# Performance work log

Hardware: AMD Instinct MI355X
Metric: run time of the kernel (lower is better)

The kernel has to match this reference:

```python
import jax, jax.numpy as jnp
import numpy as np

KSIZE = 3
COUT = 128
GC = 4

def _unfold(x, k):
    # x: [B,C,H,W] -> [B,C,k*k,H,W]; zero pad (k-1)//2, stride 1 (matches nn.Unfold ordering)
    B, C, H, W = x.shape
    p = (k - 1) // 2
    xp = jnp.pad(x, ((0, 0), (0, 0), (p, p), (p, p)))
    return jnp.stack([xp[:, :, i:i + H, j:j + W] for i in range(k) for j in range(k)], axis=2)

def _bn(x, g, b, m, v, eps=1e-5):
    # inference-mode BatchNorm along channel axis 1, any rank
    sh = (1, -1) + (1,) * (x.ndim - 2)
    return (x - m.reshape(sh)) * (g / jnp.sqrt(v + eps)).reshape(sh) + b.reshape(sh)

def setup_inputs():
    key = jax.random.key(0)
    ks = jax.random.split(key, 15)
    B, C, H, W = 4, 128, 56, 56
    mid = C // 4
    OG = COUT * GC
    s = 0.05
    return {
        'x': jax.random.normal(ks[0], (B, C, H, W), jnp.float32),
        'Wk': jax.random.normal(ks[1], (C, C), jnp.float32) * s,
        'bn1_g': jax.random.uniform(ks[2], (C,), jnp.float32, 0.5, 1.5),
        'bn1_b': jax.random.normal(ks[3], (C,), jnp.float32) * s,
        'bn1_m': jnp.zeros((C,), jnp.float32),
        'bn1_v': jnp.ones((C,), jnp.float32),
        'W1': jax.random.normal(ks[4], (mid, 2 * C), jnp.float32) * s,
        'b1': jax.random.normal(ks[5], (mid,), jnp.float32) * s,
        'bn2_g': jax.random.uniform(ks[6], (mid,), jnp.float32, 0.5, 1.5),
        'bn2_b': jax.random.normal(ks[7], (mid,), jnp.float32) * s,
        'bn2_m': jnp.zeros((mid,), jnp.float32),
        'bn2_v': jnp.ones((mid,), jnp.float32),
        'W2': jax.random.normal(ks[8], (OG, mid), jnp.float32) * s,
        'b2': jax.random.normal(ks[9], (OG,), jnp.float32) * s,
        'gn_g': jax.random.uniform(ks[10], (OG,), jnp.float32, 0.5, 1.5),
        'gn_b': jax.random.normal(ks[11], (OG,), jnp.float32) * s,
        'Wv': jax.random.normal(ks[12], (OG, C), jnp.float32) * s,
        'bnv_g': jax.random.uniform(ks[13], (OG,), jnp.float32, 0.5, 1.5),
        'bnv_b': jax.random.normal(ks[14], (OG,), jnp.float32) * s,
        'bnv_m': jnp.zeros((OG,), jnp.float32),
        'bnv_v': jnp.ones((OG,), jnp.float32),
    }

def reference(x, Wk, bn1_g, bn1_b, bn1_m, bn1_v, W1, b1, bn2_g, bn2_b, bn2_m, bn2_v,
              W2, b2, gn_g, gn_b, Wv, bnv_g, bnv_b, bnv_m, bnv_v):
    B, C, H, W = x.shape
    k2 = KSIZE * KSIZE
    # emb_K: 1x1 conv (no bias) + BN + ReLU, then local unfold
    ke = jax.nn.relu(_bn(jnp.einsum('bchw,dc->bdhw', x, Wk), bn1_g, bn1_b, bn1_m, bn1_v))
    Kp = _unfold(ke, KSIZE)                        # [B,C,k2,H,W]
    Q = jnp.broadcast_to(x[:, :, None], Kp.shape)  # repeat x over k2 (einops '(c k)')
    QK = jnp.concatenate([Q, Kp], axis=1)          # [B,2C,k2,H,W]
    # MLP: 1x1 convs act pointwise over (k2,H,W)
    h = jax.nn.relu(_bn(jnp.einsum('bcphw,mc->bmphw', QK, W1) + b1.reshape(1, -1, 1, 1, 1),
                        bn2_g, bn2_b, bn2_m, bn2_v))
    a = jnp.einsum('bmphw,om->bophw', h, W2) + b2.reshape(1, -1, 1, 1, 1)  # [B,COUT*GC,k2,H,W]
    a = a.reshape(B, COUT, GC, k2, H, W)
    # GroupNorm: num_groups=COUT -> normalize over (GC, k2, H, W) per (b, out)
    mu = a.mean(axis=(2, 3, 4, 5), keepdims=True)
    var = jnp.mean(jnp.square(a - mu), axis=(2, 3, 4, 5), keepdims=True)
    a = (a - mu) / jnp.sqrt(var + 1e-5)
    a = a * gn_g.reshape(1, COUT, GC, 1, 1, 1) + gn_b.reshape(1, COUT, GC, 1, 1, 1)
    # emb_V: 1x1 conv (no bias) + BN, then local unfold
    v = _bn(jnp.einsum('bchw,oc->bohw', x, Wv), bnv_g, bnv_b, bnv_m, bnv_v)
    V = _unfold(v, KSIZE).reshape(B, COUT, GC, k2, H, W)
    return jnp.sum(a * V, axis=(2, 3))             # [B,COUT,H,W]
```

## Files before the change

kernel.cpp:

```cpp
#include <hip/hip_runtime.h>
#include <hip/hip_bf16.h>

typedef __hip_bfloat16 bf16;
typedef __attribute__((ext_vector_type(8))) short short8;
typedef __attribute__((ext_vector_type(4))) float f32x4;

#define HWP 3136
#define WD 56
#define PW 58
#define PADP 3364
#define CC 128
#define MIDM 32
#define OGN 512
#define NB 4

enum : int {
  OFF_FLAG = 0,
  OFF_W2F  = 4,
  OFF_SC2  = OFF_W2F + OGN*MIDM,
  OFF_SH2  = OFF_SC2 + MIDM,
  OFF_B1F  = OFF_SH2 + MIDM,
  OFF_B2F  = OFF_B1F + MIDM,
  OFF_GNG  = OFF_B2F + OGN,
  OFF_GNB  = OFF_GNG + OGN,
  OFF_GPART= OFF_GNB + OGN,
  OFF_PQ   = OFF_GPART + NB*128*1056,
  OFF_SS1  = OFF_PQ + NB*OGN*2,
  OFF_SSV  = OFF_SS1 + CC*2,
  OFF_WKB  = OFF_SSV + OGN*2,
  OFF_WVB  = OFF_WKB + CC*CC/2,
  OFF_W1AB = OFF_WVB + OGN*CC/2,
  OFF_W1BB = OFF_W1AB + MIDM*CC/2,
  OFF_HQT  = OFF_W1BB + MIDM*CC/2,
  OFF_GKT  = OFF_HQT + NB*HWP*MIDM/2,
  OFF_VT   = OFF_GKT + NB*PADP*MIDM/2,
  OFF_R1   = OFF_VT + NB*PADP*OGN/2,
  OFF_XT   = OFF_R1,
  OFF_AB   = OFF_R1,
  WS_TOTAL = OFF_R1 + NB*9*HWP*MIDM/2
};

__device__ __forceinline__ float b2f(unsigned short u) {
  bf16 h; *(unsigned short*)&h = u; return __bfloat162float(h);
}
__device__ __forceinline__ unsigned short f2b(float f) {
  bf16 h = __float2bfloat16(f); return *(unsigned short*)&h;
}
__device__ __forceinline__ float ldmix(const void* p, size_t i, bool isbf) {
  return isbf ? __bfloat162float(((const bf16*)p)[i]) : ((const float*)p)[i];
}
__device__ __forceinline__ f32x4 mfma16(short8 a, short8 b, f32x4 c) {
  return __builtin_amdgcn_mfma_f32_16x16x32_bf16(a, b, c, 0, 0, 0);
}
__device__ __forceinline__ bool detect_bf(const unsigned short* xr) {
  int cnt = 0;
#pragma unroll
  for (int i = 0; i < 32; i++) {
    short8 v = *(const short8*)(xr + i*8);
#pragma unroll
    for (int j = 0; j < 8; j++) {
      int e = (((unsigned short)v[j]) >> 7) & 0xFF;
      cnt += (e >= 141) ? 1 : 0;
    }
  }
  return cnt < 8;
}

__global__ __launch_bounds__(256) void k_prep(
    const void* __restrict__ x,  const void* __restrict__ Wk,
    const void* __restrict__ bn1_g, const void* __restrict__ bn1_b,
    const void* __restrict__ bn1_m, const void* __restrict__ bn1_v,
    const void* __restrict__ W1, const void* __restrict__ b1,
    const void* __restrict__ bn2_g, const void* __restrict__ bn2_b,
    const void* __restrict__ bn2_m, const void* __restrict__ bn2_v,
    const void* __restrict__ W2, const void* __restrict__ b2,
    const void* __restrict__ gn_g, const void* __restrict__ gn_b,
    const void* __restrict__ Wv,
    const void* __restrict__ bnv_g, const void* __restrict__ bnv_b,
    const void* __restrict__ bnv_m, const void* __restrict__ bnv_v,
    float* __restrict__ ws) {
  __shared__ unsigned short tile[32*130];
  const bool isbf = detect_bf((const unsigned short*)x);
  int blk = blockIdx.x, tid = threadIdx.x;
  if (blk == 0 && tid == 0) ws[OFF_FLAG] = isbf ? 1.f : 0.f;
  int gid = blk*256 + tid, gstride = gridDim.x*256;
  unsigned short* wkb = (unsigned short*)(ws + OFF_WKB);
  unsigned short* wvb = (unsigned short*)(ws + OFF_WVB);
  unsigned short* w1ab = (unsigned short*)(ws + OFF_W1AB);
  unsigned short* w1bb = (unsigned short*)(ws + OFF_W1BB);
  float2* ss1 = (float2*)(ws + OFF_SS1);
  float2* ssv = (float2*)(ws + OFF_SSV);
  for (int i = gid; i < CC*CC; i += gstride) wkb[i] = f2b(ldmix(Wk, i, isbf));
  for (int i = gid; i < OGN*CC; i += gstride) wvb[i] = f2b(ldmix(Wv, i, isbf));
  for (int i = gid; i < MIDM*CC; i += gstride) {
    int m = i / CC, c = i % CC;
    w1ab[i] = f2b(ldmix(W1, (size_t)m*(2*CC) + c, isbf));
    w1bb[i] = f2b(ldmix(W1, (size_t)m*(2*CC) + CC + c, isbf));
  }
  for (int i = gid; i < OGN*MIDM; i += gstride) ws[OFF_W2F + i] = ldmix(W2, i, isbf);
  for (int i = gid; i < CC; i += gstride) {
    float s = ldmix(bn1_g, i, isbf) / sqrtf(ldmix(bn1_v, i, isbf) + 1e-5f);
    ss1[i] = make_float2(s, ldmix(bn1_b, i, isbf) - ldmix(bn1_m, i, isbf) * s);
  }
  for (int i = gid; i < MIDM; i += gstride) {
    float s = ldmix(bn2_g, i, isbf) / sqrtf(ldmix(bn2_v, i, isbf) + 1e-5f);
    ws[OFF_SC2 + i] = s;
    ws[OFF_SH2 + i] = ldmix(bn2_b, i, isbf) - ldmix(bn2_m, i, isbf)*s;
    ws[OFF_B1F + i] = ldmix(b1, i, isbf);
  }
  for (int i = gid; i < OGN; i += gstride) {
    float s = ldmix(bnv_g, i, isbf) / sqrtf(ldmix(bnv_v, i, isbf) + 1e-5f);
    ssv[i] = make_float2(s, ldmix(bnv_b, i, isbf) - ldmix(bnv_m, i, isbf) * s);
    ws[OFF_B2F + i] = ldmix(b2, i, isbf);
    ws[OFF_GNG + i] = ldmix(gn_g, i, isbf);
    ws[OFF_GNB + i] = ldmix(gn_b, i, isbf);
  }
  if (blk < 392) {
    int b = blk / 98, pix0 = (blk % 98)*32;
#pragma unroll
    for (int k = 0; k < 16; k++) {
      int idx = tid + k*256;
      int c = idx >> 5, pl = idx & 31;
      tile[pl*130 + c] = f2b(ldmix(x, ((size_t)b*CC + c)*HWP + pix0 + pl, isbf));
    }
    __syncthreads();
    unsigned short* xt = (unsigned short*)(ws + OFF_XT);
#pragma unroll
    for (int k = 0; k < 16; k++) {
      int idx = tid + k*256;
      int c = idx & 127, pl = idx >> 7;
      xt[((size_t)b*HWP + pix0 + pl)*CC + c] = tile[pl*130 + c];
    }
  } else {
    const int NV = 912*64, NG = NB*PADP*4;
    const short8 z = {0,0,0,0,0,0,0,0};
    unsigned short* vt = (unsigned short*)(ws + OFF_VT);
    unsigned short* gk = (unsigned short*)(ws + OFF_GKT);
    for (int u = (blk-392)*256 + tid; u < NV + NG; u += 28*256) {
      if (u < NV) {
        int bpp = u >> 6, och = u & 63;
        int b = bpp / 228, j = bpp - b*228;
        int pp;
        if (j < 58)       pp = j;
        else if (j < 116) pp = 57*PW + (j - 58);
        else if (j < 172) pp = (j - 116 + 1)*PW;
        else              pp = (j - 172 + 1)*PW + 57;
        *(short8*)(vt + ((size_t)b*PADP + pp)*OGN + och*8) = z;
      } else {
        int u2 = u - NV;
        int b = u2 / (PADP*4), rem = u2 - b*(PADP*4);
        int pp = rem >> 2, mch = rem & 3;
        *(short8*)(gk + ((size_t)b*PADP + pp)*MIDM + mch*8) = z;
      }
    }
  }
}

__global__ __launch_bounds__(256, 4) void k_mid(float* __restrict__ ws) {
  __shared__ unsigned short keL[4][16][136];
  int bid = blockIdx.x, tid = threadIdx.x;
  int w = tid >> 6, lane = tid & 63, q = lane >> 4, l16 = lane & 15;
  if (bid < 196) {
    int b = bid / 49, bx = bid - (bid/49)*49;
    int pix = bx*64 + w*16 + l16;
    const unsigned short* xt = (const unsigned short*)(ws + OFF_XT) + ((size_t)b*HWP + pix)*CC;
    short8 Bx[4];
#pragma unroll
    for (int kk = 0; kk < 4; kk++) Bx[kk] = *(const short8*)(xt + kk*32 + q*8);
    const unsigned short* wkb = (const unsigned short*)(ws + OFF_WKB);
    const float2* ss = (const float2*)(ws + OFF_SS1);
#pragma unroll
    for (int ot = 0; ot < 8; ot++) {
      int drow = ot*16 + l16;
      f32x4 c = {0.f, 0.f, 0.f, 0.f};
#pragma unroll
      for (int kk = 0; kk < 4; kk++)
        c = mfma16(*(const short8*)(wkb + (size_t)drow*CC + kk*32 + q*8), Bx[kk], c);
      int d0 = ot*16 + q*4;
      ushort4 st;
      { float2 s = ss[d0+0]; st.x = f2b(fmaxf(s.x*c[0] + s.y, 0.f)); }
      { float2 s = ss[d0+1]; st.y = f2b(fmaxf(s.x*c[1] + s.y, 0.f)); }
      { float2 s = ss[d0+2]; st.z = f2b(fmaxf(s.x*c[2] + s.y, 0.f)); }
      { float2 s = ss[d0+3]; st.w = f2b(fmaxf(s.x*c[3] + s.y, 0.f)); }
      *(ushort4*)&keL[w][l16][d0] = st;
    }
    __syncthreads();
    short8 Bk[4];
#pragma unroll
    for (int kk = 0; kk < 4; kk++) Bk[kk] = *(const short8*)&keL[w][l16][kk*32 + q*8];
    const unsigned short* w1a = (const unsigned short*)(ws + OFF_W1AB);
    const unsigned short* w1b = (const unsigned short*)(ws + OFF_W1BB);
    int h0 = pix / WD, w0 = pix - h0*WD;
    int pp = (h0+1)*PW + (w0+1);
    unsigned short* hqt = (unsigned short*)(ws + OFF_HQT) + ((size_t)b*HWP + pix)*MIDM;
    unsigned short* gkt = (unsigned short*)(ws + OFF_GKT) + ((size_t)b*PADP + pp)*MIDM;
#pragma unroll
    for (int mt = 0; mt < 2; mt++) {
      int mrow = mt*16 + l16;
      f32x4 ch = {0.f,0.f,0.f,0.f}, cg = {0.f,0.f,0.f,0.f};
#pragma unroll
      for (int kk = 0; kk < 4; kk++) {
        ch = mfma16(*(const short8*)(w1a + (size_t)mrow*CC + kk*32 + q*8), Bx[kk], ch);
        cg = mfma16(*(const short8*)(w1b + (size_t)mrow*CC + kk*32 + q*8), Bk[kk], cg);
      }
      int m0 = mt*16 + q*4;
      ushort4 sh, sg;
      sh.x = f2b(ch[0]); sh.y = f2b(ch[1]); sh.z = f2b(ch[2]); sh.w = f2b(ch[3]);
      sg.x = f2b(cg[0]); sg.y = f2b(cg[1]); sg.z = f2b(cg[2]); sg.w = f2b(cg[3]);
      *(ushort4*)(hqt + m0) = sh;
      *(ushort4*)(gkt + m0) = sg;
    }
  } else {
    int vid = bid - 196;
    int bx = vid % 49, rest = vid / 49;
    int by = rest & 3, b = rest >> 2;
    int pix = bx*64 + w*16 + l16;
    int h0 = pix / WD, w0 = pix - h0*WD;
    int pp = (h0+1)*PW + (w0+1);
    const unsigned short* xt = (const unsigned short*)(ws + OFF_XT) + ((size_t)b*HWP + pix)*CC;
    short8 B[4];
#pragma unroll
    for (int kk = 0; kk < 4; kk++) B[kk] = *(const short8*)(xt + kk*32 + q*8);
    const unsigned short* wvb = (const unsigned short*)(ws + OFF_WVB);
    const float2* ss = (const float2*)(ws + OFF_SSV);
    unsigned short* vt = (unsigned short*)(ws + OFF_VT) + ((size_t)b*PADP + pp)*OGN;
#pragma unroll
    for (int ot = 0; ot < 8; ot++) {
      int orow = by*128 + ot*16 + l16;
      f32x4 c = {0.f, 0.f, 0.f, 0.f};
#pragma unroll
      for (int kk = 0; kk < 4; kk++)
        c = mfma16(*(const short8*)(wvb + (size_t)orow*CC + kk*32 + q*8), B[kk], c);
      int o0 = by*128 + ot*16 + q*4;
      ushort4 st;
      { float2 s = ss[o0+0]; st.x = f2b(s.x*c[0] + s.y); }
      { float2 s = ss[o0+1]; st.y = f2b(s.x*c[1] + s.y); }
      { float2 s = ss[o0+2]; st.z = f2b(s.x*c[2] + s.y); }
      { float2 s = ss[o0+3]; st.w = f2b(s.x*c[3] + s.y); }
      *(ushort4*)(vt + o0) = st;
    }
  }
}

__global__ __launch_bounds__(256) void k_gramh(float* __restrict__ ws) {
  __shared__ unsigned short tileT[32][264];
  int b = blockIdx.y, bk = blockIdx.x;
  int tid = threadIdx.x;
  int w = tid >> 6, lane = tid & 63, q = lane >> 4, l16 = lane & 15;
  const int base = bk * 882;
  const unsigned short* hqt = (const unsigned short*)(ws + OFF_HQT) + (size_t)b*HWP*MIDM;
  const unsigned short* gkp = (const unsigned short*)(ws + OFF_GKT) + (size_t)b*PADP*MIDM;
  float sc2[MIDM], bas0[MIDM];
#pragma unroll
  for (int m = 0; m < MIDM; m++) {
    sc2[m] = ws[OFF_SC2 + m];
    bas0[m] = sc2[m]*ws[OFF_B1F + m] + ws[OFF_SH2 + m];
  }
  f32x4 gLL={0,0,0,0}, gLH={0,0,0,0}, gHH={0,0,0,0}, sL={0,0,0,0}, sH={0,0,0,0};
  short8 ones;
#pragma unroll
  for (int j = 0; j < 8; j++) ones[j] = (short)0x3F80;
  for (int t = 0; t < 4; t++) {
    int r = t*256 + tid;
    bool valid = r < 882;
    int R = valid ? (base + r) : 0;
    int p = R / HWP, pix = R - p*HWP;
    int h0 = pix / WD, w0 = pix - h0*WD;
    int npp = (h0 + p/3)*PW + (w0 + p - (p/3)*3);
    const unsigned short* hq = hqt + (size_t)pix*MIDM;
    const unsigned short* gk = gkp + (size_t)npp*MIDM;
#pragma unroll
    for (int ch = 0; ch < 4; ch++) {
      short8 th = *(const short8*)(hq + ch*8);
      short8 tg = *(const short8*)(gk + ch*8);
      short8 o;
#pragma unroll
      for (int j = 0; j < 8; j++) {
        int m = ch*8 + j;
        float hv = b2f((unsigned short)th[j]) + b2f((unsigned short)tg[j]);
        float v = fmaxf(sc2[m]*hv + bas0[m], 0.f);
        o[j] = valid ? (short)f2b(v) : (short)0;
      }
#pragma unroll
      for (int j = 0; j < 8; j++) tileT[ch*8 + j][tid] = (unsigned short)o[j];
    }
    __syncthreads();
#pragma unroll
    for (int cc = 0; cc < 2; cc++) {
      int c = w*2 + cc;
      short8 alo = *(const short8*)&tileT[l16][c*32 + q*8];
      short8 ahi = *(const short8*)&tileT[l16+16][c*32 + q*8];
      gLL = mfma16(alo, alo, gLL);
      gLH = mfma16(alo, ahi, gLH);
      gHH = mfma16(ahi, ahi, gHH);
      sL = mfma16(alo, ones, sL);
      sH = mfma16(ahi, ones, sH);
    }
    __syncthreads();
  }
  float* blob = ws + OFF_GPART + ((size_t)((b*32 + bk)*4 + w))*1056;
#pragma unroll
  for (int r = 0; r < 4; r++) {
    int row = q*4 + r;
    blob[row*32 + l16]             = gLL[r];
    blob[row*32 + 16 + l16]        = gLH[r];
    blob[(16 + l16)*32 + row]      = gLH[r];
    blob[(16 + row)*32 + 16 + l16] = gHH[r];
  }
  if (l16 == 0) {
#pragma unroll
    for (int r = 0; r < 4; r++) {
      blob[1024 + q*4 + r]      = sL[r];
      blob[1024 + 16 + q*4 + r] = sH[r];
    }
  }
}

__global__ __launch_bounds__(512) void k_stats(float* __restrict__ ws) {
  __shared__ float Gs[MIDM*MIDM], S1s[MIDM], saS[OGN], sqS[OGN], muS[128], invS[128];
  int b = blockIdx.x, o = threadIdx.x;
  for (int e = o; e < 1056; e += 512) {
    float s = 0.f;
    const float* pb = ws + OFF_GPART + (size_t)b*128*1056 + e;
    for (int p = 0; p < 128; p++) s += pb[(size_t)p*1056];
    if (e < 1024) Gs[e] = s; else S1s[e - 1024] = s;
  }
  __syncthreads();
  float w2[MIDM];
#pragma unroll
  for (int m = 0; m < MIDM; m++) w2[m] = ws[OFF_W2F + o*MIDM + m];
  float dotS = 0.f;
#pragma unroll
  for (int m = 0; m < MIDM; m++) dotS += w2[m] * S1s[m];
  float quad = 0.f;
  for (int a = 0; a < MIDM; a++) {
    float t = 0.f;
#pragma unroll
    for (int c = 0; c < MIDM; c++) t += Gs[a*MIDM + c] * w2[c];
    quad += w2[a] * t;
  }
  float b2o = ws[OFF_B2F + o];
  const float M = 9.f * HWP;
  saS[o] = dotS + b2o * M;
  sqS[o] = quad + 2.f*b2o*dotS + b2o*b2o*M;
  __syncthreads();
  if (o < 128) {
    float sa = saS[4*o] + saS[4*o+1] + saS[4*o+2] + saS[4*o+3];
    float sq = sqS[4*o] + sqS[4*o+1] + sqS[4*o+2] + sqS[4*o+3];
    const float invN = 1.f / (4.f * M);
    float mu = sa * invN;
    float var = sq * invN - mu*mu;
    muS[o] = mu;
    invS[o] = 1.f / sqrtf(var + 1e-5f);
  }
  __syncthreads();
  int co = o >> 2;
  float alpha = ws[OFF_GNG + o] * invS[co];
  ((float2*)(ws + OFF_PQ))[b*OGN + o] =
      make_float2(alpha, alpha*b2o + ws[OFF_GNB + o] - muS[co]*alpha);
  unsigned short* dst = (unsigned short*)(ws + OFF_AB) + ((size_t)b*OGN + o)*MIDM;
#pragma unroll
  for (int m = 0; m < MIDM; m += 4) {
    ushort4 t;
    t.x = f2b(alpha*w2[m+0]); t.y = f2b(alpha*w2[m+1]);
    t.z = f2b(alpha*w2[m+2]); t.w = f2b(alpha*w2[m+3]);
    *(ushort4*)(dst + m) = t;
  }
}

#define VST2 68
__global__ __launch_bounds__(256, 4) void k_out(const float* __restrict__ ws,
                                                void* __restrict__ outp) {
  __shared__ unsigned short tileV[256*VST2];
  int b = blockIdx.z, by = blockIdx.y;
  int bx = blockIdx.x;
  int tid = threadIdx.x;
  int w = tid >> 6, lane = tid & 63, q = lane >> 4, l16 = lane & 15;
  int pix0 = bx*128;
  int h00 = pix0 / WD, w00 = pix0 - h00*WD;
  int wstart = (h00+1)*PW + (w00+1) - (PW+1);
  const bool hasB = (bx < 24);
  int pixA = pix0 + w*16 + l16;
  float sc[8], ba[8];
#pragma unroll
  for (int j = 0; j < 8; j++) {
    int m = q*8 + j;
    sc[j] = ws[OFF_SC2 + m];
    ba[j] = sc[j]*ws[OFF_B1F + m] + ws[OFF_SH2 + m];
  }
  const unsigned short* hqt = (const unsigned short*)(ws + OFF_HQT) + (size_t)b*HWP*MIDM;
  const unsigned short* gkt = (const unsigned short*)(ws + OFF_GKT) + (size_t)b*PADP*MIDM;
  int hA = pixA / WD, wA = pixA - hA*WD;
  short8 BfA[9];
  {
    short8 th = *(const short8*)(hqt + (size_t)pixA*MIDM + q*8);
    float hv[8];
#pragma unroll
    for (int j = 0; j < 8; j++) hv[j] = b2f((unsigned short)th[j]);
    const unsigned short* gkb = gkt + ((size_t)hA*PW + wA)*MIDM + q*8;
#pragma unroll
    for (int p = 0; p < 9; p++) {
      short8 tg = *(const short8*)(gkb + (size_t)((p/3)*PW + (p - (p/3)*3))*MIDM);
#pragma unroll
      for (int j = 0; j < 8; j++)
        BfA[p][j] = (short)f2b(fmaxf(sc[j]*(hv[j] + b2f((unsigned short)tg[j])) + ba[j], 0.f));
    }
  }
  const unsigned short* vsrc = (const unsigned short*)(ws + OFF_VT)
      + (size_t)b*PADP*OGN + (size_t)by*64;
#pragma unroll
  for (int i = 0; i < 16; i++) {
    int u = i*256 + tid;
    int wp = u >> 4, col = (u & 15)*4;
    *(ushort4*)&tileV[wp*VST2 + col] =
        *(const ushort4*)(vsrc + (size_t)(wstart + wp)*OGN + col);
  }
  const bool isbf = ws[OFF_FLAG] > 0.5f;
  const float2* pq = (const float2*)(ws + OFF_PQ) + b*OGN;
  const unsigned short* ABp = (const unsigned short*)(ws + OFF_AB)
      + ((size_t)b*OGN + by*64)*MIDM;
  short8 A[4];
  f32x4 Qv[4];
#pragma unroll
  for (int ot = 0; ot < 4; ot++) {
    A[ot] = *(const short8*)(ABp + (size_t)(ot*16 + l16)*MIDM + q*8);
    int o0 = by*64 + ot*16 + q*4;
    f32x4 qv = { pq[o0+0].y, pq[o0+1].y, pq[o0+2].y, pq[o0+3].y };
    Qv[ot] = qv;
  }
  const int doff[9] = {-PW-1, -PW, -PW+1, -1, 0, 1, PW-1, PW, PW+1};
  __syncthreads();
  {
    int ppl = (hA+1)*PW + (wA+1) - wstart;
    float acc[4] = {0.f, 0.f, 0.f, 0.f};
#pragma unroll
    for (int p = 0; p < 9; p++) {
      int lp = ppl + doff[p];
      const unsigned short* vrow = &tileV[lp*VST2];
#pragma unroll
      for (int ot = 0; ot < 4; ot++) {
        f32x4 c = {0.f, 0.f, 0.f, 0.f};
        c = mfma16(A[ot], BfA[p], c);
        ushort4 vv = *(const ushort4*)(vrow + ot*16 + q*4);
        acc[ot] += (c[0] + Qv[ot][0])*b2f(vv.x) + (c[1] + Qv[ot][1])*b2f(vv.y)
                 + (c[2] + Qv[ot][2])*b2f(vv.z) + (c[3] + Qv[ot][3])*b2f(vv.w);
      }
    }
#pragma unroll
    for (int ot = 0; ot < 4; ot++) {
      int co = by*16 + ot*4 + q;
      size_t oidx = ((size_t)b*128 + co)*HWP + pixA;
      if (isbf) __builtin_nontemporal_store(f2b(acc[ot]), (unsigned short*)outp + oidx);
      else      __builtin_nontemporal_store(acc[ot], (float*)outp + oidx);
    }
  }
  if (hasB) {
    int pixB = pixA + 64;
    int hB = pixB / WD, wB = pixB - hB*WD;
    short8 BfB[9];
    {
      short8 th = *(const short8*)(hqt + (size_t)pixB*MIDM + q*8);
      float hv[8];
#pragma unroll
      for (int j = 0; j < 8; j++) hv[j] = b2f((unsigned short)th[j]);
      const unsigned short* gkb = gkt + ((size_t)hB*PW + wB)*MIDM + q*8;
#pragma unroll
      for (int p = 0; p < 9; p++) {
        short8 tg = *(const short8*)(gkb + (size_t)((p/3)*PW + (p - (p/3)*3))*MIDM);
#pragma unroll
        for (int j = 0; j < 8; j++)
          BfB[p][j] = (short)f2b(fmaxf(sc[j]*(hv[j] + b2f((unsigned short)tg[j])) + ba[j], 0.f));
      }
    }
    int ppl = (hB+1)*PW + (wB+1) - wstart;
    float acc[4] = {0.f, 0.f, 0.f, 0.f};
#pragma unroll
    for (int p = 0; p < 9; p++) {
      int lp = ppl + doff[p];
      const unsigned short* vrow = &tileV[lp*VST2];
#pragma unroll
      for (int ot = 0; ot < 4; ot++) {
        f32x4 c = {0.f, 0.f, 0.f, 0.f};
        c = mfma16(A[ot], BfB[p], c);
        ushort4 vv = *(const ushort4*)(vrow + ot*16 + q*4);
        acc[ot] += (c[0] + Qv[ot][0])*b2f(vv.x) + (c[1] + Qv[ot][1])*b2f(vv.y)
                 + (c[2] + Qv[ot][2])*b2f(vv.z) + (c[3] + Qv[ot][3])*b2f(vv.w);
      }
    }
#pragma unroll
    for (int ot = 0; ot < 4; ot++) {
      int co = by*16 + ot*4 + q;
      size_t oidx = ((size_t)b*128 + co)*HWP + pixB;
      if (isbf) __builtin_nontemporal_store(f2b(acc[ot]), (unsigned short*)outp + oidx);
      else      __builtin_nontemporal_store(acc[ot], (float*)outp + oidx);
    }
  }
}

extern "C" void kernel_launch(void* const* d_in, const int* in_sizes, int n_in,
                              void* d_out, int out_size, void* d_ws, size_t ws_size,
                              hipStream_t stream) {
  float* ws = (float*)d_ws;
  hipLaunchKernelGGL(k_prep, dim3(420), dim3(256), 0, stream,
                     d_in[0], d_in[1], d_in[2], d_in[3], d_in[4], d_in[5],
                     d_in[6], d_in[7], d_in[8], d_in[9], d_in[10], d_in[11],
                     d_in[12], d_in[13], d_in[14], d_in[15], d_in[16],
                     d_in[17], d_in[18], d_in[19], d_in[20], ws);
  hipLaunchKernelGGL(k_mid,  dim3(980),      dim3(256), 0, stream, ws);
  hipLaunchKernelGGL(k_gramh,dim3(32, 4),    dim3(256), 0, stream, ws);
  hipLaunchKernelGGL(k_stats,dim3(4),        dim3(512), 0, stream, ws);
  hipLaunchKernelGGL(k_out,  dim3(25, 8, 4), dim3(256), 0, stream, ws, d_out);
}
```

Before: 213.7 us.

## Process two 64-channel output chunks per k_out block to reuse pixel operands

Each k_out block now covers 128 output channels in two passes instead of 64, so the grid's y dimension is halved. The shared V tile doubles in width and is loaded with wider vector copies. The first pixel's relu-MLP B fragments (BfA) are computed once and reused across both channel passes, which cuts redundant gather and conversion work. In exchange, shared memory per block doubles, the launch-bounds occupancy hint drops to 2, and there are half as many blocks. BfB is still recomputed in each pass.

```diff
diff --git a/kernel.cpp b/kernel.cpp
--- a/kernel.cpp
+++ b/kernel.cpp
@@ -368,11 +368,11 @@
   }
 }
 
-#define VST2 68
-__global__ __launch_bounds__(256, 4) void k_out(const float* __restrict__ ws,
+#define VST 136
+__global__ __launch_bounds__(256, 2) void k_out(const float* __restrict__ ws,
                                                 void* __restrict__ outp) {
-  __shared__ unsigned short tileV[256*VST2];
-  int b = blockIdx.z, by = blockIdx.y;
+  __shared__ unsigned short tileV[256*VST];
+  int b = blockIdx.z, bp = blockIdx.y;
   int bx = blockIdx.x;
   int tid = threadIdx.x;
   int w = tid >> 6, lane = tid & 63, q = lane >> 4, l16 = lane & 15;
@@ -407,92 +407,94 @@
     }
   }
   const unsigned short* vsrc = (const unsigned short*)(ws + OFF_VT)
-      + (size_t)b*PADP*OGN + (size_t)by*64;
+      + (size_t)b*PADP*OGN + (size_t)bp*128;
 #pragma unroll
   for (int i = 0; i < 16; i++) {
     int u = i*256 + tid;
-    int wp = u >> 4, col = (u & 15)*4;
-    *(ushort4*)&tileV[wp*VST2 + col] =
-        *(const ushort4*)(vsrc + (size_t)(wstart + wp)*OGN + col);
+    int wp = u >> 4, col = (u & 15)*8;
+    *(short8*)&tileV[wp*VST + col] =
+        *(const short8*)(vsrc + (size_t)(wstart + wp)*OGN + col);
   }
   const bool isbf = ws[OFF_FLAG] > 0.5f;
   const float2* pq = (const float2*)(ws + OFF_PQ) + b*OGN;
-  const unsigned short* ABp = (const unsigned short*)(ws + OFF_AB)
-      + ((size_t)b*OGN + by*64)*MIDM;
-  short8 A[4];
-  f32x4 Qv[4];
-#pragma unroll
-  for (int ot = 0; ot < 4; ot++) {
-    A[ot] = *(const short8*)(ABp + (size_t)(ot*16 + l16)*MIDM + q*8);
-    int o0 = by*64 + ot*16 + q*4;
-    f32x4 qv = { pq[o0+0].y, pq[o0+1].y, pq[o0+2].y, pq[o0+3].y };
-    Qv[ot] = qv;
-  }
+  const unsigned short* ABb = (const unsigned short*)(ws + OFF_AB)
+      + ((size_t)b*OGN + bp*128)*MIDM;
   const int doff[9] = {-PW-1, -PW, -PW+1, -1, 0, 1, PW-1, PW, PW+1};
+  int pplA = (hA+1)*PW + (wA+1) - wstart;
   __syncthreads();
-  {
-    int ppl = (hA+1)*PW + (wA+1) - wstart;
-    float acc[4] = {0.f, 0.f, 0.f, 0.f};
-#pragma unroll
-    for (int p = 0; p < 9; p++) {
-      int lp = ppl + doff[p];
-      const unsigned short* vrow = &tileV[lp*VST2];
+  for (int byv = 0; byv < 2; ++byv) {
+    short8 A[4];
+    f32x4 Qv[4];
+#pragma unroll
+    for (int ot = 0; ot < 4; ot++) {
+      A[ot] = *(const short8*)(ABb + (size_t)(byv*64 + ot*16 + l16)*MIDM + q*8);
+      int o0 = bp*128 + byv*64 + ot*16 + q*4;
+      f32x4 qv = { pq[o0+0].y, pq[o0+1].y, pq[o0+2].y, pq[o0+3].y };
+      Qv[ot] = qv;
+    }
+    {
+      float acc[4] = {0.f, 0.f, 0.f, 0.f};
+#pragma unroll
+      for (int p = 0; p < 9; p++) {
+        int lp = pplA + doff[p];
+        const unsigned short* vrow = &tileV[lp*VST + byv*64];
+#pragma unroll
+        for (int ot = 0; ot < 4; ot++) {
+          f32x4 c = {0.f, 0.f, 0.f, 0.f};
+          c = mfma16(A[ot], BfA[p], c);
+          ushort4 vv = *(const ushort4*)(vrow + ot*16 + q*4);
+          acc[ot] += (c[0] + Qv[ot][0])*b2f(vv.x) + (c[1] + Qv[ot][1])*b2f(vv.y)
+                   + (c[2] + Qv[ot][2])*b2f(vv.z) + (c[3] + Qv[ot][3])*b2f(vv.w);
+        }
+      }
 #pragma unroll
       for (int ot = 0; ot < 4; ot++) {
-        f32x4 c = {0.f, 0.f, 0.f, 0.f};
-        c = mfma16(A[ot], BfA[p], c);
-        ushort4 vv = *(const ushort4*)(vrow + ot*16 + q*4);
-        acc[ot] += (c[0] + Qv[ot][0])*b2f(vv.x) + (c[1] + Qv[ot][1])*b2f(vv.y)
-                 + (c[2] + Qv[ot][2])*b2f(vv.z) + (c[3] + Qv[ot][3])*b2f(vv.w);
-      }
-    }
-#pragma unroll
-    for (int ot = 0; ot < 4; ot++) {
-      int co = by*16 + ot*4 + q;
-      size_t oidx = ((size_t)b*128 + co)*HWP + pixA;
-      if (isbf) __builtin_nontemporal_store(f2b(acc[ot]), (unsigned short*)outp + oidx);
-      else      __builtin_nontemporal_store(acc[ot], (float*)outp + oidx);
-    }
-  }
-  if (hasB) {
-    int pixB = pixA + 64;
-    int hB = pixB / WD, wB = pixB - hB*WD;
-    short8 BfB[9];
-    {
-      short8 th = *(const short8*)(hqt + (size_t)pixB*MIDM + q*8);
-      float hv[8];
-#pragma unroll
-      for (int j = 0; j < 8; j++) hv[j] = b2f((unsigned short)th[j]);
-      const unsigned short* gkb = gkt + ((size_t)hB*PW + wB)*MIDM + q*8;
+        int co = bp*32 + byv*16 + ot*4 + q;
+        size_t oidx = ((size_t)b*128 + co)*HWP + pixA;
+        if (isbf) __builtin_nontemporal_store(f2b(acc[ot]), (unsigned short*)outp + oidx);
+        else      __builtin_nontemporal_store(acc[ot], (float*)outp + oidx);
+      }
+    }
+    if (hasB) {
+      int pixB = pixA + 64;
+      int hB = pixB / WD, wB = pixB - hB*WD;
+      short8 BfB[9];
+      {
+        short8 th = *(const short8*)(hqt + (size_t)pixB*MIDM + q*8);
+        float hv[8];
+#pragma unroll
+        for (int j = 0; j < 8; j++) hv[j] = b2f((unsigned short)th[j]);
+        const unsigned short* gkb = gkt + ((size_t)hB*PW + wB)*MIDM + q*8;
+#pragma unroll
+        for (int p = 0; p < 9; p++) {
+          short8 tg = *(const short8*)(gkb + (size_t)((p/3)*PW + (p - (p/3)*3))*MIDM);
+#pragma unroll
+          for (int j = 0; j < 8; j++)
+            BfB[p][j] = (short)f2b(fmaxf(sc[j]*(hv[j] + b2f((unsigned short)tg[j])) + ba[j], 0.f));
+        }
+      }
+      int ppl = (hB+1)*PW + (wB+1) - wstart;
+      float acc[4] = {0.f, 0.f, 0.f, 0.f};
 #pragma unroll
       for (int p = 0; p < 9; p++) {
-        short8 tg = *(const short8*)(gkb + (size_t)((p/3)*PW + (p - (p/3)*3))*MIDM);
-#pragma unroll
-        for (int j = 0; j < 8; j++)
-          BfB[p][j] = (short)f2b(fmaxf(sc[j]*(hv[j] + b2f((unsigned short)tg[j])) + ba[j], 0.f));
-      }
-    }
-    int ppl = (hB+1)*PW + (wB+1) - wstart;
-    float acc[4] = {0.f, 0.f, 0.f, 0.f};
-#pragma unroll
-    for (int p = 0; p < 9; p++) {
-      int lp = ppl + doff[p];
-      const unsigned short* vrow = &tileV[lp*VST2];
+        int lp = ppl + doff[p];
+        const unsigned short* vrow = &tileV[lp*VST + byv*64];
+#pragma unroll
+        for (int ot = 0; ot < 4; ot++) {
+          f32x4 c = {0.f, 0.f, 0.f, 0.f};
+          c = mfma16(A[ot], BfB[p], c);
+          ushort4 vv = *(const ushort4*)(vrow + ot*16 + q*4);
+          acc[ot] += (c[0] + Qv[ot][0])*b2f(vv.x) + (c[1] + Qv[ot][1])*b2f(vv.y)
+                   + (c[2] + Qv[ot][2])*b2f(vv.z) + (c[3] + Qv[ot][3])*b2f(vv.w);
+        }
+      }
 #pragma unroll
       for (int ot = 0; ot < 4; ot++) {
-        f32x4 c = {0.f, 0.f, 0.f, 0.f};
-        c = mfma16(A[ot], BfB[p], c);
-        ushort4 vv = *(const ushort4*)(vrow + ot*16 + q*4);
-        acc[ot] += (c[0] + Qv[ot][0])*b2f(vv.x) + (c[1] + Qv[ot][1])*b2f(vv.y)
-                 + (c[2] + Qv[ot][2])*b2f(vv.z) + (c[3] + Qv[ot][3])*b2f(vv.w);
-      }
-    }
-#pragma unroll
-    for (int ot = 0; ot < 4; ot++) {
-      int co = by*16 + ot*4 + q;
-      size_t oidx = ((size_t)b*128 + co)*HWP + pixB;
-      if (isbf) __builtin_nontemporal_store(f2b(acc[ot]), (unsigned short*)outp + oidx);
-      else      __builtin_nontemporal_store(acc[ot], (float*)outp + oidx);
+        int co = bp*32 + byv*16 + ot*4 + q;
+        size_t oidx = ((size_t)b*128 + co)*HWP + pixB;
+        if (isbf) __builtin_nontemporal_store(f2b(acc[ot]), (unsigned short*)outp + oidx);
+        else      __builtin_nontemporal_store(acc[ot], (float*)outp + oidx);
+      }
     }
   }
 }
@@ -509,5 +511,5 @@
   hipLaunchKernelGGL(k_mid,  dim3(980),      dim3(256), 0, stream, ws);
   hipLaunchKernelGGL(k_gramh,dim3(32, 4),    dim3(256), 0, stream, ws);
   hipLaunchKernelGGL(k_stats,dim3(4),        dim3(512), 0, stream, ws);
-  hipLaunchKernelGGL(k_out,  dim3(25, 8, 4), dim3(256), 0, stream, ws, d_out);
-}
+  hipLaunchKernelGGL(k_out,  dim3(25, 4, 4), dim3(256), 0, stream, ws, d_out);
+}
```

Result: faster. 192.9 us (-9.7%).
